# Kernel tuning notes

Measured on AMD Instinct MI355X. Metric: run time of the kernel, lower is better.

Reference implementation:

```python
import jax, jax.numpy as jnp
import numpy as np

B, D_IN, H, T_EMB = 16384, 256, 512, 16


def _lin_params(key, out_dim, in_dim, bias):
    k1, k2 = jax.random.split(key)
    s = 1.0 / np.sqrt(in_dim)
    W = jax.random.uniform(k1, (out_dim, in_dim), jnp.float32, -s, s)
    b = jax.random.uniform(k2, (out_dim,), jnp.float32, -s, s) if bias else None
    return W, b


def setup_inputs() -> dict:
    key = jax.random.key(0)
    ks = jax.random.split(key, 20)
    x = jax.random.normal(ks[0], (B, D_IN), jnp.float32)
    h = jax.random.normal(ks[1], (B, H), jnp.float32)
    c_prev = jax.random.normal(ks[2], (B, H), jnp.float32)
    delt = jax.random.uniform(ks[3], (B, T_EMB), jnp.float32)

    W_ix, b_ix = _lin_params(ks[4], H, D_IN, True)
    W_ih, _ = _lin_params(ks[5], H, H, False)
    W_ic, _ = _lin_params(ks[6], H, H, False)
    W_fx, b_fx = _lin_params(ks[7], H, D_IN, True)
    W_fh, _ = _lin_params(ks[8], H, H, False)
    W_fc, _ = _lin_params(ks[9], H, H, False)
    W_tx, b_tx = _lin_params(ks[10], H, D_IN, True)
    W_tt, _ = _lin_params(ks[11], H, T_EMB, False)
    W_cx, b_cx = _lin_params(ks[12], H, D_IN, True)
    W_ch, _ = _lin_params(ks[13], H, H, False)
    W_ox, b_ox = _lin_params(ks[14], H, D_IN, True)
    W_oh, _ = _lin_params(ks[15], H, H, False)
    W_oc, _ = _lin_params(ks[16], H, H, False)
    W_ot, _ = _lin_params(ks[17], H, T_EMB, False)

    return dict(x=x, h=h, c_prev=c_prev, delt=delt,
                W_ix=W_ix, b_ix=b_ix, W_ih=W_ih, W_ic=W_ic,
                W_fx=W_fx, b_fx=b_fx, W_fh=W_fh, W_fc=W_fc,
                W_tx=W_tx, b_tx=b_tx, W_tt=W_tt,
                W_cx=W_cx, b_cx=b_cx, W_ch=W_ch,
                W_ox=W_ox, b_ox=b_ox, W_oh=W_oh, W_oc=W_oc, W_ot=W_ot)


def reference(x, h, c_prev, delt,
              W_ix, b_ix, W_ih, W_ic,
              W_fx, b_fx, W_fh, W_fc,
              W_tx, b_tx, W_tt,
              W_cx, b_cx, W_ch,
              W_ox, b_ox, W_oh, W_oc, W_ot):
    sig, tanh = jax.nn.sigmoid, jnp.tanh
    # input gate
    i = sig(x @ W_ix.T + b_ix + h @ W_ih.T + c_prev @ W_ic.T)
    # forget gate
    f = sig(x @ W_fx.T + b_fx + h @ W_fh.T + c_prev @ W_fc.T)
    # time gate: note inner sigmoid on the time-delta projection
    T = sig(x @ W_tx.T + b_tx + sig(delt @ W_tt.T))
    # candidate cell and new cell state
    k = tanh(x @ W_cx.T + b_cx + h @ W_ch.T)
    c_next = i * T * k + f * c_prev
    # output gate
    o = sig(x @ W_ox.T + b_ox + delt @ W_ot.T + h @ W_oh.T + c_prev @ W_oc.T)
    h_next = o * tanh(c_next)
    return (h_next, c_next, T)
```

## Files before the change

kernel.cpp:

```cpp
#include <hip/hip_runtime.h>
#include <cstdint>

#define B_SZ   16384
#define H_SZ   512
#define DIN    256
#define TEMB   16
#define KP     1344
#define KPB    1344
#define BH     8388608L
#define SLOT   24576
#define TSLOT  20480
#define GSTR   688128

typedef __attribute__((ext_vector_type(4))) float f32x4;
typedef __attribute__((ext_vector_type(4))) int   i32x4;

typedef const __attribute__((address_space(1))) unsigned int gu32_t;
typedef __attribute__((address_space(3)))       unsigned int lu32_t;

__device__ __forceinline__ void gld16(const void* g, void* l) {
  __builtin_amdgcn_global_load_lds((gu32_t*)(uintptr_t)g,
                                   (lu32_t*)(unsigned int)(uintptr_t)l, 16, 0, 0);
}

__device__ __forceinline__ float sigm(float v)  { return 1.0f / (1.0f + __expf(-v)); }
__device__ __forceinline__ float tanhx(float v) { return 2.0f / (1.0f + __expf(-2.0f * v)) - 1.0f; }

__device__ __forceinline__ signed char q8(float v, float inv) {
  int q = __float2int_rn(v * inv);
  q = (q > 127) ? 127 : (q < -127 ? -127 : q);
  return (signed char)q;
}

__global__ void prep_a8_kernel(const float* __restrict__ x, const float* __restrict__ h,
                               const float* __restrict__ c, const float* __restrict__ dl,
                               signed char* __restrict__ Ap, float* __restrict__ sa) {
  const int tid  = threadIdx.x;
  const int lane = tid & 63;
  const int m    = blockIdx.x * 4 + (tid >> 6);
  float4 v[6];
  float lmax = 0.f;
#pragma unroll
  for (int i = 0; i < 6; ++i) {
    const int k4 = (i * 64 + lane) * 4;
    float4 t = make_float4(0.f, 0.f, 0.f, 0.f);
    if (k4 < 256)       t = *(const float4*)(x  + (size_t)m * DIN  + k4);
    else if (k4 < 768)  t = *(const float4*)(h  + (size_t)m * H_SZ + (k4 - 256));
    else if (k4 < 1280) t = *(const float4*)(c  + (size_t)m * H_SZ + (k4 - 768));
    else if (k4 < 1296) t = *(const float4*)(dl + (size_t)m * TEMB + (k4 - 1280));
    v[i] = t;
    lmax = fmaxf(lmax, fmaxf(fmaxf(fabsf(t.x), fabsf(t.y)), fmaxf(fabsf(t.z), fabsf(t.w))));
  }
#pragma unroll
  for (int s = 1; s < 64; s <<= 1)
    lmax = fmaxf(lmax, __shfl_xor(lmax, s));
  const float smax = fmaxf(lmax, 1e-20f);
  const float inv  = 127.0f / smax;
  if (lane == 0) sa[m] = smax * (1.0f / 127.0f);
#pragma unroll
  for (int i = 0; i < 6; ++i) {
    const int k4 = (i * 64 + lane) * 4;
    if (k4 < KP) {
      char4 o;
      o.x = q8(v[i].x, inv); o.y = q8(v[i].y, inv);
      o.z = q8(v[i].z, inv); o.w = q8(v[i].w, inv);
      *(char4*)(Ap + (size_t)m * KPB + k4) = o;
    }
  }
}

__global__ void prep_w8_kernel(const float* __restrict__ Wix, const float* __restrict__ Wih, const float* __restrict__ Wic,
                               const float* __restrict__ Wfx, const float* __restrict__ Wfh, const float* __restrict__ Wfc,
                               const float* __restrict__ Wtx, const float* __restrict__ Wtt,
                               const float* __restrict__ Wcx, const float* __restrict__ Wch,
                               const float* __restrict__ Wox, const float* __restrict__ Woh,
                               const float* __restrict__ Woc, const float* __restrict__ Wot,
                               signed char* __restrict__ Wp, float* __restrict__ sw) {
  __shared__ float row[KP];
  __shared__ float red[256];
  const int R   = blockIdx.x;
  const int g   = R >> 9;
  const int n   = R & 511;
  const int tid = threadIdx.x;
  float lmax = 0.f;
  for (int i = tid; i < KP / 4; i += 256) {
    const int k4 = i * 4;
    const float* src = nullptr; long o = 0;
    if (g == 0) {
      if (k4 < 256)       { src = Wix; o = (long)n * 256 + k4; }
      else if (k4 < 768)  { src = Wih; o = (long)n * 512 + (k4 - 256); }
      else if (k4 < 1280) { src = Wic; o = (long)n * 512 + (k4 - 768); }
    } else if (g == 1) {
      if (k4 < 256)       { src = Wfx; o = (long)n * 256 + k4; }
      else if (k4 < 768)  { src = Wfh; o = (long)n * 512 + (k4 - 256); }
      else if (k4 < 1280) { src = Wfc; o = (long)n * 512 + (k4 - 768); }
    } else if (g == 2) {
      if (k4 < 256)       { src = Wtx; o = (long)n * 256 + k4; }
    } else if (g == 3) {
      if (k4 < 256)       { src = Wcx; o = (long)n * 256 + k4; }
      else if (k4 < 768)  { src = Wch; o = (long)n * 512 + (k4 - 256); }
    } else if (g == 4) {
      if (k4 < 256)       { src = Wox; o = (long)n * 256 + k4; }
      else if (k4 < 768)  { src = Woh; o = (long)n * 512 + (k4 - 256); }
      else if (k4 < 1280) { src = Woc; o = (long)n * 512 + (k4 - 768); }
      else if (k4 < 1296) { src = Wot; o = (long)n * 16 + (k4 - 1280); }
    } else {
      if (k4 >= 1280 && k4 < 1296) { src = Wtt; o = (long)n * 16 + (k4 - 1280); }
    }
    float4 v = make_float4(0.f, 0.f, 0.f, 0.f);
    if (src) v = *(const float4*)(src + o);
    *(float4*)(row + k4) = v;
    lmax = fmaxf(lmax, fmaxf(fmaxf(fabsf(v.x), fabsf(v.y)), fmaxf(fabsf(v.z), fabsf(v.w))));
  }
  red[tid] = lmax;
  __syncthreads();
  for (int s = 128; s > 0; s >>= 1) {
    if (tid < s) red[tid] = fmaxf(red[tid], red[tid + s]);
    __syncthreads();
  }
  const float smax = fmaxf(red[0], 1e-20f);
  const float inv  = 127.0f / smax;
  if (tid == 0) sw[R] = smax * (1.0f / 127.0f);
  for (int i = tid; i < KP / 4; i += 256) {
    const int k4 = i * 4;
    char4 o;
    o.x = q8(row[k4],     inv); o.y = q8(row[k4 + 1], inv);
    o.z = q8(row[k4 + 2], inv); o.w = q8(row[k4 + 3], inv);
    *(char4*)(Wp + (size_t)R * KPB + k4) = o;
  }
}


__device__ __forceinline__ void stage(char* lds, int sb, int ht,
                                      const char* sAb, const char* sWb, int wid) {
  const unsigned kb = (unsigned)ht * 64u;
  gld16(sAb + kb,              lds + sb + wid * 2048);
  gld16(sAb + kb + 16u * KPB,  lds + sb + wid * 2048 + 1024);
  const int r = wid >> 1, c = wid & 1;
  const int g = r + (r >> 1);
  gld16(sWb + (unsigned)g * GSTR + (unsigned)c * (16u * KPB) + kb,
        lds + sb + 16384 + r * 2048 + c * 1024);
}

template<unsigned CM, int NW, bool ST>
__device__ __forceinline__ void phase(char* lds, int rs, int ws, int ht,
    const char* sAb, const char* sWb, int wid, int aro, int wro, i32x4 acc[4][4]) {
  asm volatile("s_waitcnt vmcnt(%0)" :: "i"(NW) : "memory");
  __builtin_amdgcn_s_barrier();
  __builtin_amdgcn_sched_barrier(0);
  const char* base = lds + rs;
  i32x4 a[4];
#pragma unroll
  for (int i = 0; i < 4; ++i)
    a[i] = *(const i32x4*)(base + aro + i * 1024);
  i32x4 b[4];
#pragma unroll
  for (int r = 0; r < 4; ++r)
    if (CM & (1u << r))
      b[r] = *(const i32x4*)(base + 16384 + r * 2048 + wro);
  if (ST) stage(lds, ws, ht, sAb, sWb, wid);
  asm volatile("s_waitcnt lgkmcnt(0)" ::: "memory");
  __builtin_amdgcn_sched_barrier(0);
  __builtin_amdgcn_s_setprio(1);
#pragma unroll
  for (int r = 0; r < 4; ++r) {
    if (CM & (1u << r)) {
#pragma unroll
      for (int i = 0; i < 4; ++i)
        acc[r][i] = __builtin_amdgcn_mfma_i32_16x16x64_i8(a[i], b[r], acc[r][i], 0, 0, 0);
    }
  }
  __builtin_amdgcn_s_setprio(0);
}

__global__ __launch_bounds__(512, 4) void lstm_main(
    const signed char* __restrict__ Ap, const signed char* __restrict__ Wp,
    const float* __restrict__ sa, const float* __restrict__ sw,
    const float* __restrict__ c_prev,
    const float* __restrict__ b_ix, const float* __restrict__ b_fx,
    const float* __restrict__ b_cx, const float* __restrict__ b_ox,
    float* __restrict__ out)
{
  __shared__ __align__(16) char lds[3 * SLOT];

  const int tid  = threadIdx.x;
  const int lane = tid & 63;
  const int wid  = tid >> 6;

  const int bid = blockIdx.x;
  const int xcd = bid & 7;
  const int idx = bid >> 3;
  const int cb  = (xcd << 1) | (idx & 1);
  const int rb  = idx >> 1;
  const unsigned brow = (unsigned)rb * 256u;
  const int bcol = cb * 32;

  const int wr  = (wid >> 1) * 64;
  const int wcg = (wid & 1) * 16;
  const int lrow = lane & 15;
  const int kgrp = lane >> 4;

  i32x4 acc[4][4];
  {
    i32x4 z = {0, 0, 0, 0};
#pragma unroll
    for (int g = 0; g < 4; ++g)
#pragma unroll
      for (int i = 0; i < 4; ++i) acc[g][i] = z;
  }

  const int sread = ((kgrp + (lrow >> 1)) & 3) << 4;
  const int aro = (wr + lrow) * 64 + sread;
  const int wro = (wcg + lrow) * 64 + sread;

  const int l4 = lane >> 2;
  const int kslot = (((lane & 3) - ((lane >> 3) & 3)) & 3) << 4;
  const char* sAb = (const char*)Ap + (size_t)(brow + wid * 32 + l4) * KPB + kslot;
  const char* sWb = (const char*)Wp + (size_t)(bcol + l4) * KPB + kslot;

  stage(lds, 0,    0, sAb, sWb, wid);
  stage(lds, SLOT, 1, sAb, sWb, wid);

  int rs = 0;
#define PH(CMv, NWv, STv, HT) do {                                             \
    int ws = (rs >= SLOT) ? rs - SLOT : rs + 2 * SLOT;                         \
    phase<CMv, NWv, STv>(lds, rs, ws, HT, sAb, sWb, wid, aro, wro, acc);       \
    rs = (rs == 2 * SLOT) ? 0 : rs + SLOT;                                     \
  } while (0)

#pragma unroll 1
  for (int h = 0; h < 11; ++h) PH(0xF, 3, true, h + 2);
  PH(0xF, 3, true, 13);
#pragma unroll 1
  for (int h = 12; h < 19; ++h) PH(0xB, 3, true, h + 2);
  PH(0xB, 3, false, 0);
  PH(0x8, 0, false, 0);
#undef PH

  const float* Tvp = out + 2 * BH;
  const int n = bcol + wcg + lrow;
  const float bi = b_ix[n], bff = b_fx[n], bc = b_cx[n], bo = b_ox[n];
  const float s0 = sw[0 * 512 + n], s1 = sw[1 * 512 + n];
  const float s3 = sw[3 * 512 + n], s4 = sw[4 * 512 + n];
  const int rbase = kgrp * 4;
#pragma unroll
  for (int i = 0; i < 4; ++i) {
    const int m0 = (int)brow + wr + 16 * i + rbase;
    const float4 sa4 = *(const float4*)(sa + m0);
#pragma unroll
    for (int r = 0; r < 4; ++r) {
      const long m   = m0 + r;
      const long off = m * H_SZ + n;
      const float sr = (r == 0) ? sa4.x : (r == 1) ? sa4.y : (r == 2) ? sa4.z : sa4.w;
      const float iv = sigm((float)acc[0][i][r] * sr * s0 + bi);
      const float fv = sigm((float)acc[1][i][r] * sr * s1 + bff);
      const float kv = tanhx((float)acc[2][i][r] * sr * s3 + bc);
      const float ov = sigm((float)acc[3][i][r] * sr * s4 + bo);
      const float Tv = Tvp[off];
      const float cp = c_prev[off];
      const float cn = iv * Tv * kv + fv * cp;
      out[off]      = ov * tanhx(cn);
      out[BH + off] = cn;
    }
  }
}

template<unsigned SMASK>
__device__ __forceinline__ void stage_t(char* lds, int sb, int ht,
                                        const char* sAb, const char* sWb, int wid) {
  const unsigned kb = (unsigned)ht * 64u;
  gld16(sAb + kb,              lds + sb + wid * 2048);
  gld16(sAb + kb + 16u * KPB,  lds + sb + wid * 2048 + 1024);
  if (wid < 4) {
    const int r = wid >> 1, c = wid & 1;
    if (SMASK & (1u << r)) {
      const int g = (r == 0) ? 2 : 5;
      gld16(sWb + (unsigned)g * GSTR + (unsigned)c * (16u * KPB) + kb,
            lds + sb + 16384 + r * 2048 + c * 1024);
    }
  }
}

template<unsigned CM>
__device__ __forceinline__ void comp_t(const char* lds, int sb, int aro, int wro,
                                       i32x4 acc[2][4]) {
  const char* base = lds + sb;
  i32x4 a[4];
#pragma unroll
  for (int i = 0; i < 4; ++i)
    a[i] = *(const i32x4*)(base + aro + i * 1024);
#pragma unroll
  for (int r = 0; r < 2; ++r) {
    if (CM & (1u << r)) {
      i32x4 b = *(const i32x4*)(base + 16384 + r * 2048 + wro);
#pragma unroll
      for (int i = 0; i < 4; ++i)
        acc[r][i] = __builtin_amdgcn_mfma_i32_16x16x64_i8(a[i], b, acc[r][i], 0, 0, 0);
    }
  }
}

__global__ __launch_bounds__(512, 4) void tgate_kernel(
    const signed char* __restrict__ Ap, const signed char* __restrict__ Wp,
    const float* __restrict__ sa, const float* __restrict__ sw,
    const float* __restrict__ b_tx, float* __restrict__ out)
{
  __shared__ __align__(16) char lds[2 * TSLOT];

  const int tid  = threadIdx.x;
  const int lane = tid & 63;
  const int wid  = tid >> 6;

  const int bid = blockIdx.x;
  const int xcd = bid & 7;
  const int idx = bid >> 3;
  const int cb  = (xcd << 1) | (idx & 1);
  const int rb  = idx >> 1;
  const unsigned brow = (unsigned)rb * 256u;
  const int bcol = cb * 32;

  const int wr  = (wid >> 1) * 64;
  const int wcg = (wid & 1) * 16;
  const int lrow = lane & 15;
  const int kgrp = lane >> 4;

  i32x4 acc[2][4];
  {
    i32x4 z = {0, 0, 0, 0};
#pragma unroll
    for (int g = 0; g < 2; ++g)
#pragma unroll
      for (int i = 0; i < 4; ++i) acc[g][i] = z;
  }

  const int sread = ((kgrp + (lrow >> 1)) & 3) << 4;
  const int aro = (wr + lrow) * 64 + sread;
  const int wro = (wcg + lrow) * 64 + sread;

  const int l4 = lane >> 2;
  const int kslot = (((lane & 3) - ((lane >> 3) & 3)) & 3) << 4;
  const char* sAb = (const char*)Ap + (size_t)(brow + wid * 32 + l4) * KPB + kslot;
  const char* sWb = (const char*)Wp + (size_t)(bcol + l4) * KPB + kslot;

  stage_t<0x1>(lds, 0, 0, sAb, sWb, wid);
  __syncthreads();
  stage_t<0x1>(lds, TSLOT, 1, sAb, sWb, wid);
  comp_t<0x1>(lds, 0, aro, wro, acc);
  __syncthreads();
  stage_t<0x1>(lds, 0, 2, sAb, sWb, wid);
  comp_t<0x1>(lds, TSLOT, aro, wro, acc);
  __syncthreads();
  stage_t<0x1>(lds, TSLOT, 3, sAb, sWb, wid);
  comp_t<0x1>(lds, 0, aro, wro, acc);
  __syncthreads();
  stage_t<0x2>(lds, 0, 20, sAb, sWb, wid);
  comp_t<0x1>(lds, TSLOT, aro, wro, acc);
  __syncthreads();
  comp_t<0x2>(lds, 0, aro, wro, acc);

  const int n = bcol + wcg + lrow;
  const float bt = b_tx[n];
  const float s2 = sw[2 * 512 + n], s5 = sw[5 * 512 + n];
  const int rbase = kgrp * 4;
#pragma unroll
  for (int i = 0; i < 4; ++i) {
    const int m0 = (int)brow + wr + 16 * i + rbase;
    const float4 sa4 = *(const float4*)(sa + m0);
#pragma unroll
    for (int r = 0; r < 4; ++r) {
      const long off = (long)(m0 + r) * H_SZ + n;
      const float sr = (r == 0) ? sa4.x : (r == 1) ? sa4.y : (r == 2) ? sa4.z : sa4.w;
      const float inner = sigm((float)acc[1][i][r] * sr * s5);
      out[2 * BH + off] = sigm((float)acc[0][i][r] * sr * s2 + bt + inner);
    }
  }
}

extern "C" void kernel_launch(void* const* d_in, const int* in_sizes, int n_in,
                              void* d_out, int out_size, void* d_ws, size_t ws_size,
                              hipStream_t stream) {
  const float* x      = (const float*)d_in[0];
  const float* h      = (const float*)d_in[1];
  const float* c_prev = (const float*)d_in[2];
  const float* dl     = (const float*)d_in[3];
  const float* W_ix = (const float*)d_in[4];
  const float* b_ix = (const float*)d_in[5];
  const float* W_ih = (const float*)d_in[6];
  const float* W_ic = (const float*)d_in[7];
  const float* W_fx = (const float*)d_in[8];
  const float* b_fx = (const float*)d_in[9];
  const float* W_fh = (const float*)d_in[10];
  const float* W_fc = (const float*)d_in[11];
  const float* W_tx = (const float*)d_in[12];
  const float* b_tx = (const float*)d_in[13];
  const float* W_tt = (const float*)d_in[14];
  const float* W_cx = (const float*)d_in[15];
  const float* b_cx = (const float*)d_in[16];
  const float* W_ch = (const float*)d_in[17];
  const float* W_ox = (const float*)d_in[18];
  const float* b_ox = (const float*)d_in[19];
  const float* W_oh = (const float*)d_in[20];
  const float* W_oc = (const float*)d_in[21];
  const float* W_ot = (const float*)d_in[22];

  signed char* Ap8 = (signed char*)d_ws;
  signed char* Wp8 = (signed char*)d_ws + (size_t)B_SZ * KPB;
  float* sa = (float*)((char*)d_ws + (size_t)B_SZ * KPB + 6L * H_SZ * KPB);
  float* sw = sa + B_SZ;

  prep_a8_kernel<<<B_SZ / 4, 256, 0, stream>>>(x, h, c_prev, dl, Ap8, sa);
  prep_w8_kernel<<<6 * H_SZ, 256, 0, stream>>>(
      W_ix, W_ih, W_ic, W_fx, W_fh, W_fc, W_tx, W_tt, W_cx, W_ch,
      W_ox, W_oh, W_oc, W_ot, Wp8, sw);

  tgate_kernel<<<1024, 512, 0, stream>>>(Ap8, Wp8, sa, sw, b_tx, (float*)d_out);

  lstm_main<<<1024, 512, 0, stream>>>(Ap8, Wp8, sa, sw, c_prev,
                                      b_ix, b_fx, b_cx, b_ox,
                                      (float*)d_out);
}
```

Baseline: 115.7 us.

## Load int8 weight fragments directly from global memory and merge prep kernels

The main GEMM loop no longer stages the weight tile through LDS. Each lane now reads its B fragments straight from global memory, which shrinks the LDS ring slot from 24 KB to 16 KB and drops the lgkmcnt wait for B reads. The two quantization prep kernels are also merged into one launch to save a kernel launch. The trade-off is that direct global weight loads can add latency and uncached traffic inside the MFMA loop, though the smaller LDS footprint may raise occupancy.

```diff
diff --git a/kernel.cpp b/kernel.cpp
--- a/kernel.cpp
+++ b/kernel.cpp
@@ -8,7 +8,7 @@
 #define KP     1344
 #define KPB    1344
 #define BH     8388608L
-#define SLOT   24576
+#define SLOT   16384
 #define TSLOT  20480
 #define GSTR   688128
 
@@ -32,56 +32,56 @@
   return (signed char)q;
 }
 
-__global__ void prep_a8_kernel(const float* __restrict__ x, const float* __restrict__ h,
-                               const float* __restrict__ c, const float* __restrict__ dl,
-                               signed char* __restrict__ Ap, float* __restrict__ sa) {
-  const int tid  = threadIdx.x;
-  const int lane = tid & 63;
-  const int m    = blockIdx.x * 4 + (tid >> 6);
-  float4 v[6];
-  float lmax = 0.f;
-#pragma unroll
-  for (int i = 0; i < 6; ++i) {
-    const int k4 = (i * 64 + lane) * 4;
-    float4 t = make_float4(0.f, 0.f, 0.f, 0.f);
-    if (k4 < 256)       t = *(const float4*)(x  + (size_t)m * DIN  + k4);
-    else if (k4 < 768)  t = *(const float4*)(h  + (size_t)m * H_SZ + (k4 - 256));
-    else if (k4 < 1280) t = *(const float4*)(c  + (size_t)m * H_SZ + (k4 - 768));
-    else if (k4 < 1296) t = *(const float4*)(dl + (size_t)m * TEMB + (k4 - 1280));
-    v[i] = t;
-    lmax = fmaxf(lmax, fmaxf(fmaxf(fabsf(t.x), fabsf(t.y)), fmaxf(fabsf(t.z), fabsf(t.w))));
-  }
-#pragma unroll
-  for (int s = 1; s < 64; s <<= 1)
-    lmax = fmaxf(lmax, __shfl_xor(lmax, s));
-  const float smax = fmaxf(lmax, 1e-20f);
-  const float inv  = 127.0f / smax;
-  if (lane == 0) sa[m] = smax * (1.0f / 127.0f);
-#pragma unroll
-  for (int i = 0; i < 6; ++i) {
-    const int k4 = (i * 64 + lane) * 4;
-    if (k4 < KP) {
-      char4 o;
-      o.x = q8(v[i].x, inv); o.y = q8(v[i].y, inv);
-      o.z = q8(v[i].z, inv); o.w = q8(v[i].w, inv);
-      *(char4*)(Ap + (size_t)m * KPB + k4) = o;
-    }
-  }
-}
-
-__global__ void prep_w8_kernel(const float* __restrict__ Wix, const float* __restrict__ Wih, const float* __restrict__ Wic,
-                               const float* __restrict__ Wfx, const float* __restrict__ Wfh, const float* __restrict__ Wfc,
-                               const float* __restrict__ Wtx, const float* __restrict__ Wtt,
-                               const float* __restrict__ Wcx, const float* __restrict__ Wch,
-                               const float* __restrict__ Wox, const float* __restrict__ Woh,
-                               const float* __restrict__ Woc, const float* __restrict__ Wot,
-                               signed char* __restrict__ Wp, float* __restrict__ sw) {
+__global__ void prep_kernel(const float* __restrict__ x, const float* __restrict__ h,
+                            const float* __restrict__ c, const float* __restrict__ dl,
+                            const float* __restrict__ Wix, const float* __restrict__ Wih, const float* __restrict__ Wic,
+                            const float* __restrict__ Wfx, const float* __restrict__ Wfh, const float* __restrict__ Wfc,
+                            const float* __restrict__ Wtx, const float* __restrict__ Wtt,
+                            const float* __restrict__ Wcx, const float* __restrict__ Wch,
+                            const float* __restrict__ Wox, const float* __restrict__ Woh,
+                            const float* __restrict__ Woc, const float* __restrict__ Wot,
+                            signed char* __restrict__ Ap, float* __restrict__ sa,
+                            signed char* __restrict__ Wp, float* __restrict__ sw) {
   __shared__ float row[KP];
   __shared__ float red[256];
-  const int R   = blockIdx.x;
-  const int g   = R >> 9;
-  const int n   = R & 511;
   const int tid = threadIdx.x;
+  if (blockIdx.x < 4096) {
+    const int lane = tid & 63;
+    const int m    = blockIdx.x * 4 + (tid >> 6);
+    float4 v[6];
+    float lmax = 0.f;
+#pragma unroll
+    for (int i = 0; i < 6; ++i) {
+      const int k4 = (i * 64 + lane) * 4;
+      float4 t = make_float4(0.f, 0.f, 0.f, 0.f);
+      if (k4 < 256)       t = *(const float4*)(x  + (size_t)m * DIN  + k4);
+      else if (k4 < 768)  t = *(const float4*)(h  + (size_t)m * H_SZ + (k4 - 256));
+      else if (k4 < 1280) t = *(const float4*)(c  + (size_t)m * H_SZ + (k4 - 768));
+      else if (k4 < 1296) t = *(const float4*)(dl + (size_t)m * TEMB + (k4 - 1280));
+      v[i] = t;
+      lmax = fmaxf(lmax, fmaxf(fmaxf(fabsf(t.x), fabsf(t.y)), fmaxf(fabsf(t.z), fabsf(t.w))));
+    }
+#pragma unroll
+    for (int s = 1; s < 64; s <<= 1)
+      lmax = fmaxf(lmax, __shfl_xor(lmax, s));
+    const float smax = fmaxf(lmax, 1e-20f);
+    const float inv  = 127.0f / smax;
+    if (lane == 0) sa[m] = smax * (1.0f / 127.0f);
+#pragma unroll
+    for (int i = 0; i < 6; ++i) {
+      const int k4 = (i * 64 + lane) * 4;
+      if (k4 < KP) {
+        char4 o;
+        o.x = q8(v[i].x, inv); o.y = q8(v[i].y, inv);
+        o.z = q8(v[i].z, inv); o.w = q8(v[i].w, inv);
+        *(char4*)(Ap + (size_t)m * KPB + k4) = o;
+      }
+    }
+    return;
+  }
+  const int R = blockIdx.x - 4096;
+  const int g = R >> 9;
+  const int n = R & 511;
   float lmax = 0.f;
   for (int i = tid; i < KP / 4; i += 256) {
     const int k4 = i * 4;
@@ -131,21 +131,17 @@
 }
 
 
-__device__ __forceinline__ void stage(char* lds, int sb, int ht,
-                                      const char* sAb, const char* sWb, int wid) {
+__device__ __forceinline__ void stageA(char* lds, int sb, int ht,
+                                       const char* sAb, int wid) {
   const unsigned kb = (unsigned)ht * 64u;
-  gld16(sAb + kb,              lds + sb + wid * 2048);
-  gld16(sAb + kb + 16u * KPB,  lds + sb + wid * 2048 + 1024);
-  const int r = wid >> 1, c = wid & 1;
-  const int g = r + (r >> 1);
-  gld16(sWb + (unsigned)g * GSTR + (unsigned)c * (16u * KPB) + kb,
-        lds + sb + 16384 + r * 2048 + c * 1024);
-}
-
-template<unsigned CM, int NW, bool ST>
+  gld16(sAb + kb,             lds + sb + wid * 2048);
+  gld16(sAb + kb + 16u * KPB, lds + sb + wid * 2048 + 1024);
+}
+
+template<unsigned CM, int NWE, bool ST>
 __device__ __forceinline__ void phase(char* lds, int rs, int ws, int ht,
-    const char* sAb, const char* sWb, int wid, int aro, int wro, i32x4 acc[4][4]) {
-  asm volatile("s_waitcnt vmcnt(%0)" :: "i"(NW) : "memory");
+    const char* sAb, const char* wbase, int h, int wid, int aro, i32x4 acc[4][4]) {
+  asm volatile("s_waitcnt vmcnt(%0)" :: "i"(NWE) : "memory");
   __builtin_amdgcn_s_barrier();
   __builtin_amdgcn_sched_barrier(0);
   const char* base = lds + rs;
@@ -153,13 +149,13 @@
 #pragma unroll
   for (int i = 0; i < 4; ++i)
     a[i] = *(const i32x4*)(base + aro + i * 1024);
+  const size_t kb = (size_t)h * 64;
   i32x4 b[4];
-#pragma unroll
-  for (int r = 0; r < 4; ++r)
-    if (CM & (1u << r))
-      b[r] = *(const i32x4*)(base + 16384 + r * 2048 + wro);
-  if (ST) stage(lds, ws, ht, sAb, sWb, wid);
-  asm volatile("s_waitcnt lgkmcnt(0)" ::: "memory");
+  if (CM & 1u) b[0] = *(const i32x4*)(wbase + 0 * (size_t)GSTR + kb);
+  if (CM & 2u) b[1] = *(const i32x4*)(wbase + 1 * (size_t)GSTR + kb);
+  if (CM & 4u) b[2] = *(const i32x4*)(wbase + 3 * (size_t)GSTR + kb);
+  if (CM & 8u) b[3] = *(const i32x4*)(wbase + 4 * (size_t)GSTR + kb);
+  if (ST) stageA(lds, ws, ht, sAb, wid);
   __builtin_amdgcn_sched_barrier(0);
   __builtin_amdgcn_s_setprio(1);
 #pragma unroll
@@ -211,30 +207,28 @@
 
   const int sread = ((kgrp + (lrow >> 1)) & 3) << 4;
   const int aro = (wr + lrow) * 64 + sread;
-  const int wro = (wcg + lrow) * 64 + sread;
 
   const int l4 = lane >> 2;
   const int kslot = (((lane & 3) - ((lane >> 3) & 3)) & 3) << 4;
-  const char* sAb = (const char*)Ap + (size_t)(brow + wid * 32 + l4) * KPB + kslot;
-  const char* sWb = (const char*)Wp + (size_t)(bcol + l4) * KPB + kslot;
-
-  stage(lds, 0,    0, sAb, sWb, wid);
-  stage(lds, SLOT, 1, sAb, sWb, wid);
+  const char* sAb   = (const char*)Ap + (size_t)(brow + wid * 32 + l4) * KPB + kslot;
+  const char* wbase = (const char*)Wp + (size_t)(bcol + wcg + lrow) * KPB + kgrp * 16;
+
+  stageA(lds, 0,    0, sAb, wid);
+  stageA(lds, SLOT, 1, sAb, wid);
 
   int rs = 0;
-#define PH(CMv, NWv, STv, HT) do {                                             \
+#define PH(CMv, NWEv, STv, HT, H) do {                                         \
     int ws = (rs >= SLOT) ? rs - SLOT : rs + 2 * SLOT;                         \
-    phase<CMv, NWv, STv>(lds, rs, ws, HT, sAb, sWb, wid, aro, wro, acc);       \
+    phase<CMv, NWEv, STv>(lds, rs, ws, HT, sAb, wbase, H, wid, aro, acc);      \
     rs = (rs == 2 * SLOT) ? 0 : rs + SLOT;                                     \
   } while (0)
 
 #pragma unroll 1
-  for (int h = 0; h < 11; ++h) PH(0xF, 3, true, h + 2);
-  PH(0xF, 3, true, 13);
+  for (int h = 0; h < 12; ++h) PH(0xF, 2, true, h + 2, h);
 #pragma unroll 1
-  for (int h = 12; h < 19; ++h) PH(0xB, 3, true, h + 2);
-  PH(0xB, 3, false, 0);
-  PH(0x8, 0, false, 0);
+  for (int h = 12; h < 19; ++h) PH(0xB, 2, true, h + 2, h);
+  PH(0xB, 2, false, 0, 19);
+  PH(0x8, 0, false, 0, 20);
 #undef PH
 
   const float* Tvp = out + 2 * BH;
@@ -408,10 +402,10 @@
   float* sa = (float*)((char*)d_ws + (size_t)B_SZ * KPB + 6L * H_SZ * KPB);
   float* sw = sa + B_SZ;
 
-  prep_a8_kernel<<<B_SZ / 4, 256, 0, stream>>>(x, h, c_prev, dl, Ap8, sa);
-  prep_w8_kernel<<<6 * H_SZ, 256, 0, stream>>>(
+  prep_kernel<<<4096 + 3072, 256, 0, stream>>>(
+      x, h, c_prev, dl,
       W_ix, W_ih, W_ic, W_fx, W_fh, W_fc, W_tx, W_tt, W_cx, W_ch,
-      W_ox, W_oh, W_oc, W_ot, Wp8, sw);
+      W_ox, W_oh, W_oc, W_ot, Ap8, sa, Wp8, sw);
 
   tgate_kernel<<<1024, 512, 0, stream>>>(Ap8, Wp8, sa, sw, b_tx, (float*)d_out);
 
```

After: 135.0 us. 16.6% more time.

## Merge prep kernels into one launch and enlarge tgate tile to 512 rows

Applied to the files above, without the earlier changes.

Combines the activation and weight int8 quantisation kernels into a single launch, with block index selecting the role, to save one kernel launch and its tail. The T-gate GEMM kernel now handles 512 rows per block with each wave covering 64 rows and both 16-column halves, so grid size halves and each staged weight tile is reused across more MFMAs. The larger LDS slot and doubled accumulators raise register and LDS pressure, which may reduce occupancy.

```diff
diff --git a/kernel.cpp b/kernel.cpp
--- a/kernel.cpp
+++ b/kernel.cpp
@@ -9,7 +9,7 @@
 #define KPB    1344
 #define BH     8388608L
 #define SLOT   24576
-#define TSLOT  20480
+#define TSLOT  36864
 #define GSTR   688128
 
 typedef __attribute__((ext_vector_type(4))) float f32x4;
@@ -32,56 +32,56 @@
   return (signed char)q;
 }
 
-__global__ void prep_a8_kernel(const float* __restrict__ x, const float* __restrict__ h,
-                               const float* __restrict__ c, const float* __restrict__ dl,
-                               signed char* __restrict__ Ap, float* __restrict__ sa) {
-  const int tid  = threadIdx.x;
-  const int lane = tid & 63;
-  const int m    = blockIdx.x * 4 + (tid >> 6);
-  float4 v[6];
-  float lmax = 0.f;
-#pragma unroll
-  for (int i = 0; i < 6; ++i) {
-    const int k4 = (i * 64 + lane) * 4;
-    float4 t = make_float4(0.f, 0.f, 0.f, 0.f);
-    if (k4 < 256)       t = *(const float4*)(x  + (size_t)m * DIN  + k4);
-    else if (k4 < 768)  t = *(const float4*)(h  + (size_t)m * H_SZ + (k4 - 256));
-    else if (k4 < 1280) t = *(const float4*)(c  + (size_t)m * H_SZ + (k4 - 768));
-    else if (k4 < 1296) t = *(const float4*)(dl + (size_t)m * TEMB + (k4 - 1280));
-    v[i] = t;
-    lmax = fmaxf(lmax, fmaxf(fmaxf(fabsf(t.x), fabsf(t.y)), fmaxf(fabsf(t.z), fabsf(t.w))));
-  }
-#pragma unroll
-  for (int s = 1; s < 64; s <<= 1)
-    lmax = fmaxf(lmax, __shfl_xor(lmax, s));
-  const float smax = fmaxf(lmax, 1e-20f);
-  const float inv  = 127.0f / smax;
-  if (lane == 0) sa[m] = smax * (1.0f / 127.0f);
-#pragma unroll
-  for (int i = 0; i < 6; ++i) {
-    const int k4 = (i * 64 + lane) * 4;
-    if (k4 < KP) {
-      char4 o;
-      o.x = q8(v[i].x, inv); o.y = q8(v[i].y, inv);
-      o.z = q8(v[i].z, inv); o.w = q8(v[i].w, inv);
-      *(char4*)(Ap + (size_t)m * KPB + k4) = o;
-    }
-  }
-}
-
-__global__ void prep_w8_kernel(const float* __restrict__ Wix, const float* __restrict__ Wih, const float* __restrict__ Wic,
-                               const float* __restrict__ Wfx, const float* __restrict__ Wfh, const float* __restrict__ Wfc,
-                               const float* __restrict__ Wtx, const float* __restrict__ Wtt,
-                               const float* __restrict__ Wcx, const float* __restrict__ Wch,
-                               const float* __restrict__ Wox, const float* __restrict__ Woh,
-                               const float* __restrict__ Woc, const float* __restrict__ Wot,
-                               signed char* __restrict__ Wp, float* __restrict__ sw) {
+__global__ void prep_kernel(const float* __restrict__ x, const float* __restrict__ h,
+                            const float* __restrict__ c, const float* __restrict__ dl,
+                            const float* __restrict__ Wix, const float* __restrict__ Wih, const float* __restrict__ Wic,
+                            const float* __restrict__ Wfx, const float* __restrict__ Wfh, const float* __restrict__ Wfc,
+                            const float* __restrict__ Wtx, const float* __restrict__ Wtt,
+                            const float* __restrict__ Wcx, const float* __restrict__ Wch,
+                            const float* __restrict__ Wox, const float* __restrict__ Woh,
+                            const float* __restrict__ Woc, const float* __restrict__ Wot,
+                            signed char* __restrict__ Ap, float* __restrict__ sa,
+                            signed char* __restrict__ Wp, float* __restrict__ sw) {
   __shared__ float row[KP];
   __shared__ float red[256];
-  const int R   = blockIdx.x;
-  const int g   = R >> 9;
-  const int n   = R & 511;
   const int tid = threadIdx.x;
+  if (blockIdx.x < 4096) {
+    const int lane = tid & 63;
+    const int m    = blockIdx.x * 4 + (tid >> 6);
+    float4 v[6];
+    float lmax = 0.f;
+#pragma unroll
+    for (int i = 0; i < 6; ++i) {
+      const int k4 = (i * 64 + lane) * 4;
+      float4 t = make_float4(0.f, 0.f, 0.f, 0.f);
+      if (k4 < 256)       t = *(const float4*)(x  + (size_t)m * DIN  + k4);
+      else if (k4 < 768)  t = *(const float4*)(h  + (size_t)m * H_SZ + (k4 - 256));
+      else if (k4 < 1280) t = *(const float4*)(c  + (size_t)m * H_SZ + (k4 - 768));
+      else if (k4 < 1296) t = *(const float4*)(dl + (size_t)m * TEMB + (k4 - 1280));
+      v[i] = t;
+      lmax = fmaxf(lmax, fmaxf(fmaxf(fabsf(t.x), fabsf(t.y)), fmaxf(fabsf(t.z), fabsf(t.w))));
+    }
+#pragma unroll
+    for (int s = 1; s < 64; s <<= 1)
+      lmax = fmaxf(lmax, __shfl_xor(lmax, s));
+    const float smax = fmaxf(lmax, 1e-20f);
+    const float inv  = 127.0f / smax;
+    if (lane == 0) sa[m] = smax * (1.0f / 127.0f);
+#pragma unroll
+    for (int i = 0; i < 6; ++i) {
+      const int k4 = (i * 64 + lane) * 4;
+      if (k4 < KP) {
+        char4 o;
+        o.x = q8(v[i].x, inv); o.y = q8(v[i].y, inv);
+        o.z = q8(v[i].z, inv); o.w = q8(v[i].w, inv);
+        *(char4*)(Ap + (size_t)m * KPB + k4) = o;
+      }
+    }
+    return;
+  }
+  const int R = blockIdx.x - 4096;
+  const int g = R >> 9;
+  const int n = R & 511;
   float lmax = 0.f;
   for (int i = tid; i < KP / 4; i += 256) {
     const int k4 = i * 4;
@@ -265,39 +265,38 @@
   }
 }
 
-template<unsigned SMASK>
 __device__ __forceinline__ void stage_t(char* lds, int sb, int ht,
-                                        const char* sAb, const char* sWb, int wid) {
+                                        const char* sAb, const char* sWt,
+                                        const char* sWu, int wid) {
   const unsigned kb = (unsigned)ht * 64u;
-  gld16(sAb + kb,              lds + sb + wid * 2048);
-  gld16(sAb + kb + 16u * KPB,  lds + sb + wid * 2048 + 1024);
-  if (wid < 4) {
-    const int r = wid >> 1, c = wid & 1;
-    if (SMASK & (1u << r)) {
-      const int g = (r == 0) ? 2 : 5;
-      gld16(sWb + (unsigned)g * GSTR + (unsigned)c * (16u * KPB) + kb,
-            lds + sb + 16384 + r * 2048 + c * 1024);
-    }
-  }
-}
-
-template<unsigned CM>
-__device__ __forceinline__ void comp_t(const char* lds, int sb, int aro, int wro,
-                                       i32x4 acc[2][4]) {
+#pragma unroll
+  for (int j = 0; j < 4; ++j)
+    gld16(sAb + kb + (unsigned)j * (16u * KPB), lds + sb + (wid * 4 + j) * 1024);
+  if (wid < 2)      gld16(sWt + kb, lds + sb + 32768 + wid * 1024);
+  else if (wid < 4) gld16(sWu + kb, lds + sb + 32768 + 2048 + (wid - 2) * 1024);
+}
+
+__device__ __forceinline__ void comp_t(const char* lds, int sb, int wid,
+                                       int lrow, int sread, i32x4 acc[2][4][2]) {
   const char* base = lds + sb;
   i32x4 a[4];
 #pragma unroll
-  for (int i = 0; i < 4; ++i)
-    a[i] = *(const i32x4*)(base + aro + i * 1024);
-#pragma unroll
-  for (int r = 0; r < 2; ++r) {
-    if (CM & (1u << r)) {
-      i32x4 b = *(const i32x4*)(base + 16384 + r * 2048 + wro);
-#pragma unroll
-      for (int i = 0; i < 4; ++i)
-        acc[r][i] = __builtin_amdgcn_mfma_i32_16x16x64_i8(a[i], b, acc[r][i], 0, 0, 0);
-    }
-  }
+  for (int mi = 0; mi < 4; ++mi)
+    a[mi] = *(const i32x4*)(base + (wid * 64 + mi * 16 + lrow) * 64 + sread);
+  i32x4 b[2][2];
+#pragma unroll
+  for (int g = 0; g < 2; ++g)
+#pragma unroll
+    for (int cf = 0; cf < 2; ++cf)
+      b[g][cf] = *(const i32x4*)(base + 32768 + g * 2048 + (cf * 16 + lrow) * 64 + sread);
+#pragma unroll
+  for (int g = 0; g < 2; ++g)
+#pragma unroll
+    for (int mi = 0; mi < 4; ++mi)
+#pragma unroll
+      for (int cf = 0; cf < 2; ++cf)
+        acc[g][mi][cf] = __builtin_amdgcn_mfma_i32_16x16x64_i8(a[mi], b[g][cf],
+                                                               acc[g][mi][cf], 0, 0, 0);
 }
 
 __global__ __launch_bounds__(512, 4) void tgate_kernel(
@@ -316,62 +315,63 @@
   const int idx = bid >> 3;
   const int cb  = (xcd << 1) | (idx & 1);
   const int rb  = idx >> 1;
-  const unsigned brow = (unsigned)rb * 256u;
+  const unsigned brow = (unsigned)rb * 512u;
   const int bcol = cb * 32;
 
-  const int wr  = (wid >> 1) * 64;
-  const int wcg = (wid & 1) * 16;
   const int lrow = lane & 15;
   const int kgrp = lane >> 4;
 
-  i32x4 acc[2][4];
+  i32x4 acc[2][4][2];
   {
     i32x4 z = {0, 0, 0, 0};
 #pragma unroll
     for (int g = 0; g < 2; ++g)
 #pragma unroll
-      for (int i = 0; i < 4; ++i) acc[g][i] = z;
+      for (int mi = 0; mi < 4; ++mi) { acc[g][mi][0] = z; acc[g][mi][1] = z; }
   }
 
   const int sread = ((kgrp + (lrow >> 1)) & 3) << 4;
-  const int aro = (wr + lrow) * 64 + sread;
-  const int wro = (wcg + lrow) * 64 + sread;
 
   const int l4 = lane >> 2;
   const int kslot = (((lane & 3) - ((lane >> 3) & 3)) & 3) << 4;
-  const char* sAb = (const char*)Ap + (size_t)(brow + wid * 32 + l4) * KPB + kslot;
-  const char* sWb = (const char*)Wp + (size_t)(bcol + l4) * KPB + kslot;
-
-  stage_t<0x1>(lds, 0, 0, sAb, sWb, wid);
-  __syncthreads();
-  stage_t<0x1>(lds, TSLOT, 1, sAb, sWb, wid);
-  comp_t<0x1>(lds, 0, aro, wro, acc);
-  __syncthreads();
-  stage_t<0x1>(lds, 0, 2, sAb, sWb, wid);
-  comp_t<0x1>(lds, TSLOT, aro, wro, acc);
-  __syncthreads();
-  stage_t<0x1>(lds, TSLOT, 3, sAb, sWb, wid);
-  comp_t<0x1>(lds, 0, aro, wro, acc);
-  __syncthreads();
-  stage_t<0x2>(lds, 0, 20, sAb, sWb, wid);
-  comp_t<0x1>(lds, TSLOT, aro, wro, acc);
-  __syncthreads();
-  comp_t<0x2>(lds, 0, aro, wro, acc);
-
-  const int n = bcol + wcg + lrow;
-  const float bt = b_tx[n];
-  const float s2 = sw[2 * 512 + n], s5 = sw[5 * 512 + n];
-  const int rbase = kgrp * 4;
-#pragma unroll
-  for (int i = 0; i < 4; ++i) {
-    const int m0 = (int)brow + wr + 16 * i + rbase;
-    const float4 sa4 = *(const float4*)(sa + m0);
-#pragma unroll
-    for (int r = 0; r < 4; ++r) {
-      const long off = (long)(m0 + r) * H_SZ + n;
-      const float sr = (r == 0) ? sa4.x : (r == 1) ? sa4.y : (r == 2) ? sa4.z : sa4.w;
-      const float inner = sigm((float)acc[1][i][r] * sr * s5);
-      out[2 * BH + off] = sigm((float)acc[0][i][r] * sr * s2 + bt + inner);
+  const char* sAb = (const char*)Ap + (size_t)(brow + wid * 64 + l4) * KPB + kslot;
+  const char* sWt = (const char*)Wp + 2 * (size_t)GSTR
+                    + (size_t)(bcol + (wid & 1) * 16 + l4) * KPB + kslot;
+  const char* sWu = (const char*)Wp + 5 * (size_t)GSTR
+                    + (size_t)(bcol + (wid & 1) * 16 + l4) * KPB + kslot;
+
+  stage_t(lds, 0, 0, sAb, sWt, sWu, wid);
+  __syncthreads();
+  stage_t(lds, TSLOT, 1, sAb, sWt, sWu, wid);
+  comp_t(lds, 0, wid, lrow, sread, acc);
+  __syncthreads();
+  stage_t(lds, 0, 2, sAb, sWt, sWu, wid);
+  comp_t(lds, TSLOT, wid, lrow, sread, acc);
+  __syncthreads();
+  stage_t(lds, TSLOT, 3, sAb, sWt, sWu, wid);
+  comp_t(lds, 0, wid, lrow, sread, acc);
+  __syncthreads();
+  stage_t(lds, 0, 20, sAb, sWt, sWu, wid);
+  comp_t(lds, TSLOT, wid, lrow, sread, acc);
+  __syncthreads();
+  comp_t(lds, 0, wid, lrow, sread, acc);
+
+#pragma unroll
+  for (int cf = 0; cf < 2; ++cf) {
+    const int n = bcol + cf * 16 + lrow;
+    const float bt = b_tx[n];
+    const float s2 = sw[2 * 512 + n], s5 = sw[5 * 512 + n];
+#pragma unroll
+    for (int mi = 0; mi < 4; ++mi) {
+      const int m0 = (int)brow + wid * 64 + mi * 16 + kgrp * 4;
+      const float4 sa4 = *(const float4*)(sa + m0);
+#pragma unroll
+      for (int r = 0; r < 4; ++r) {
+        const long off = (long)(m0 + r) * H_SZ + n;
+        const float sr = (r == 0) ? sa4.x : (r == 1) ? sa4.y : (r == 2) ? sa4.z : sa4.w;
+        const float inner = sigm((float)acc[1][mi][cf][r] * sr * s5);
+        out[2 * BH + off] = sigm((float)acc[0][mi][cf][r] * sr * s2 + bt + inner);
+      }
     }
   }
 }
@@ -408,12 +408,12 @@
   float* sa = (float*)((char*)d_ws + (size_t)B_SZ * KPB + 6L * H_SZ * KPB);
   float* sw = sa + B_SZ;
 
-  prep_a8_kernel<<<B_SZ / 4, 256, 0, stream>>>(x, h, c_prev, dl, Ap8, sa);
-  prep_w8_kernel<<<6 * H_SZ, 256, 0, stream>>>(
+  prep_kernel<<<4096 + 3072, 256, 0, stream>>>(
+      x, h, c_prev, dl,
       W_ix, W_ih, W_ic, W_fx, W_fh, W_fc, W_tx, W_tt, W_cx, W_ch,
-      W_ox, W_oh, W_oc, W_ot, Wp8, sw);
-
-  tgate_kernel<<<1024, 512, 0, stream>>>(Ap8, Wp8, sa, sw, b_tx, (float*)d_out);
+      W_ox, W_oh, W_oc, W_ot, Ap8, sa, Wp8, sw);
+
+  tgate_kernel<<<512, 512, 0, stream>>>(Ap8, Wp8, sa, sw, b_tx, (float*)d_out);
 
   lstm_main<<<1024, 512, 0, stream>>>(Ap8, Wp8, sa, sw, c_prev,
                                       b_ix, b_fx, b_cx, b_ox,
```

Result: no change. 117.8 us (+1.8%).
